# Kernel optimization log

Measured on AMD Instinct MI355X. Metric: run time of the kernel, lower is better.

## Reference

```python
import jax, jax.numpy as jnp
import numpy as np

TEMPERATURE = 0.07  # module init default
CHUNK = 2048        # row tile size, mirrors the triton tiling (never materialize full NxN)


def _normalize(x):
    # F.normalize(x, dim=1): x / max(||x||_2, eps)
    n = jnp.linalg.norm(x, axis=1, keepdims=True)
    return x / jnp.maximum(n, 1e-12)


def setup_inputs() -> dict:
    key = jax.random.key(0)
    k1, k2 = jax.random.split(key)
    N, D = 16384, 256
    return {
        "text_features": jax.random.normal(k1, (N, D), dtype=jnp.float32),
        "image_features": jax.random.normal(k2, (N, D), dtype=jnp.float32),
    }


def reference(text_features, image_features):
    X = _normalize(text_features)   # [N, D]
    Y = _normalize(image_features)  # [N, D]
    inv_t = 1.0 / TEMPERATURE
    n, d = X.shape
    Xc = X.reshape(n // CHUNK, CHUNK, d)

    def row_sum_exp(xc):
        # exp2(S*log2(e)/t - log2(e)/t) == exp((S - 1)/t); S = xc @ Y^T
        S = (jnp.einsum('id,jd->ij', xc, Y) - 1.0) * inv_t  # [CHUNK, N]
        return jnp.sum(jnp.exp(S), axis=1)                   # [CHUNK]

    # tiled accumulation of row-wise sum of exponentials (never holds NxN)
    sum_exp_row = jax.lax.map(row_sum_exp, Xc).reshape(n)   # [N]

    # diagonal (positive-pair) logits: Sv = (x_i . y_i - 1)/t
    Sv = (jnp.sum(X * Y, axis=1) - 1.0) * inv_t
    logits = jnp.log(jnp.exp(Sv) / sum_exp_row)
    return -jnp.mean(logits)
```

## Files before the change

kernel.cpp:

```cpp
#include <hip/hip_runtime.h>
#include <hip/hip_bf16.h>
#include <stdint.h>

#define D_DIM 256
#define INV_T 14.285714285714286f

#define BM 256
#define BN 256
#define BK 32
#define NSTEP (D_DIM / BK)

typedef __bf16 bf16x8 __attribute__((ext_vector_type(8)));
typedef float f32x16 __attribute__((ext_vector_type(16)));

__global__ __launch_bounds__(256) void lit_normalize(
    const float* __restrict__ X, const float* __restrict__ Y,
    __hip_bfloat16* __restrict__ Xb, __hip_bfloat16* __restrict__ Yb,
    float* __restrict__ Sv, float* __restrict__ rowsum)
{
    const int l = threadIdx.x & 63;
    const int row = blockIdx.x * 4 + (threadIdx.x >> 6);
    const size_t base = (size_t)row * D_DIM;
    const float4 x = ((const float4*)(X + base))[l];
    const float4 y = ((const float4*)(Y + base))[l];
    float nx = x.x * x.x + x.y * x.y + x.z * x.z + x.w * x.w;
    float ny = y.x * y.x + y.y * y.y + y.z * y.z + y.w * y.w;
    float dt = x.x * y.x + x.y * y.y + x.z * y.z + x.w * y.w;
    #pragma unroll
    for (int o = 1; o < 64; o <<= 1) {
        nx += __shfl_xor(nx, o);
        ny += __shfl_xor(ny, o);
        dt += __shfl_xor(dt, o);
    }
    const float ivx = 1.0f / fmaxf(sqrtf(nx), 1e-12f);
    const float ivy = 1.0f / fmaxf(sqrtf(ny), 1e-12f);

    __hip_bfloat16 hx0 = __float2bfloat16(x.x * ivx), hx1 = __float2bfloat16(x.y * ivx);
    __hip_bfloat16 hx2 = __float2bfloat16(x.z * ivx), hx3 = __float2bfloat16(x.w * ivx);
    __hip_bfloat16 hy0 = __float2bfloat16(y.x * ivy), hy1 = __float2bfloat16(y.y * ivy);
    __hip_bfloat16 hy2 = __float2bfloat16(y.z * ivy), hy3 = __float2bfloat16(y.w * ivy);
    ushort4 px, py;
    px.x = *(unsigned short*)&hx0; px.y = *(unsigned short*)&hx1;
    px.z = *(unsigned short*)&hx2; px.w = *(unsigned short*)&hx3;
    py.x = *(unsigned short*)&hy0; py.y = *(unsigned short*)&hy1;
    py.z = *(unsigned short*)&hy2; py.w = *(unsigned short*)&hy3;
    ((ushort4*)(Xb + base))[l] = px;
    ((ushort4*)(Yb + base))[l] = py;

    if (l == 0) {
        Sv[row] = (dt * ivx * ivy - 1.0f) * INV_T;
        rowsum[row] = 0.0f;
    }
}

__global__ __launch_bounds__(512, 2) void lit_gemm_rowsum(
    const __hip_bfloat16* __restrict__ Xb, const __hip_bfloat16* __restrict__ Yb,
    float* __restrict__ rowsum)
{
    __shared__ char lds[2 * 32768];

    const int tid = (int)threadIdx.x;
    const int l   = tid & 63;
    const int w   = tid >> 6;
    const int wi  = w >> 2;
    const int wj  = w & 3;

    const int nx  = (int)gridDim.x;
    const int bid = (int)blockIdx.y * nx + (int)blockIdx.x;
    const int cpx = (nx * (int)gridDim.y) >> 3;
    const int logical = (bid & 7) * cpx + (bid >> 3);
    const int bi = logical / nx;
    const int bj = logical % nx;
    const int iBase = bi * BM;
    const int jBase = bj * BN;

    f32x16 acc[2][4];
    #pragma unroll
    for (int a = 0; a < 2; ++a)
        #pragma unroll
        for (int b = 0; b < 4; ++b)
            #pragma unroll
            for (int r = 0; r < 16; ++r)
                acc[a][b][r] = 0.f;

    const int rq = l >> 2;
    const int sl = l & 3;
    const char* src[4];
    int dst[4];
    #pragma unroll
    for (int c = 0; c < 4; ++c) {
        const int g    = w * 4 + c;
        const int isY  = g >> 4;
        const int r16  = (g & 15) * 16;
        const int row  = r16 + rq;
        const int slot = sl ^ ((row >> 1) & 3);
        const char* base = isY ? (const char*)Yb + (size_t)jBase * (D_DIM * 2)
                               : (const char*)Xb + (size_t)iBase * (D_DIM * 2);
        src[c] = base + (size_t)row * (D_DIM * 2) + slot * 16;
        dst[c] = isY * 16384 + r16 * 64;
    }

#define STAGE(buf, t)                                                              \
    {                                                                              \
        _Pragma("unroll")                                                          \
        for (int c = 0; c < 4; ++c)                                                \
            __builtin_amdgcn_global_load_lds(                                      \
                (const __attribute__((address_space(1))) void*)(src[c] + (t) * (BK * 2)), \
                (__attribute__((address_space(3))) void*)(lds + (buf) * 32768 + dst[c]),  \
                16, 0, 0);                                                         \
    }

    STAGE(0, 0);
    __syncthreads();

    #pragma unroll
    for (int t = 0; t < NSTEP; ++t) {
        const char* Xs = lds + (t & 1) * 32768;
        const char* Ys = Xs + 16384;
        const int lr = l & 31;

        bf16x8 af[2][2], bg[2][4];
        #pragma unroll
        for (int kk = 0; kk < 2; ++kk) {
            const int sx = ((kk * 2 + (l >> 5)) ^ ((l >> 1) & 3)) * 16;
            af[kk][0] = *(const bf16x8*)(Ys + (wj * 64 +  0 + lr) * 64 + sx);
            af[kk][1] = *(const bf16x8*)(Ys + (wj * 64 + 32 + lr) * 64 + sx);
            bg[kk][0] = *(const bf16x8*)(Xs + (wi * 128 +  0 + lr) * 64 + sx);
            bg[kk][1] = *(const bf16x8*)(Xs + (wi * 128 + 32 + lr) * 64 + sx);
            bg[kk][2] = *(const bf16x8*)(Xs + (wi * 128 + 64 + lr) * 64 + sx);
            bg[kk][3] = *(const bf16x8*)(Xs + (wi * 128 + 96 + lr) * 64 + sx);
        }

        if (t < NSTEP - 1) STAGE((t + 1) & 1, t + 1);

        #pragma unroll
        for (int kk = 0; kk < 2; ++kk) {
            acc[0][0] = __builtin_amdgcn_mfma_f32_32x32x16_bf16(af[kk][0], bg[kk][0], acc[0][0], 0, 0, 0);
            acc[0][1] = __builtin_amdgcn_mfma_f32_32x32x16_bf16(af[kk][0], bg[kk][1], acc[0][1], 0, 0, 0);
            acc[0][2] = __builtin_amdgcn_mfma_f32_32x32x16_bf16(af[kk][0], bg[kk][2], acc[0][2], 0, 0, 0);
            acc[0][3] = __builtin_amdgcn_mfma_f32_32x32x16_bf16(af[kk][0], bg[kk][3], acc[0][3], 0, 0, 0);
            acc[1][0] = __builtin_amdgcn_mfma_f32_32x32x16_bf16(af[kk][1], bg[kk][0], acc[1][0], 0, 0, 0);
            acc[1][1] = __builtin_amdgcn_mfma_f32_32x32x16_bf16(af[kk][1], bg[kk][1], acc[1][1], 0, 0, 0);
            acc[1][2] = __builtin_amdgcn_mfma_f32_32x32x16_bf16(af[kk][1], bg[kk][2], acc[1][2], 0, 0, 0);
            acc[1][3] = __builtin_amdgcn_mfma_f32_32x32x16_bf16(af[kk][1], bg[kk][3], acc[1][3], 0, 0, 0);
        }

        __syncthreads();
    }

    float part[4];
    #pragma unroll
    for (int fi = 0; fi < 4; ++fi) {
        float s = 0.f;
        #pragma unroll
        for (int fj = 0; fj < 2; ++fj)
            #pragma unroll
            for (int r = 0; r < 16; ++r)
                s += __expf(fmaf(acc[fj][fi][r], INV_T, -INV_T));
        s += __shfl_xor(s, 32);
        part[fi] = s;
    }
    float (*rowpart4)[BM] = (float (*)[BM])lds;
    if (l < 32) {
        #pragma unroll
        for (int fi = 0; fi < 4; ++fi)
            rowpart4[wj][wi * 128 + fi * 32 + l] = part[fi];
    }
    __syncthreads();
    if (tid < BM) {
        const float v = rowpart4[0][tid] + rowpart4[1][tid]
                      + rowpart4[2][tid] + rowpart4[3][tid];
        atomicAdd(&rowsum[iBase + tid], v);
    }
}

__global__ __launch_bounds__(1024) void lit_finish(
    const float* __restrict__ Sv, const float* __restrict__ rowsum,
    float* __restrict__ out, int N)
{
    float s = 0.f;
    for (int i = threadIdx.x; i < N; i += 1024)
        s += Sv[i] - __logf(rowsum[i]);
    #pragma unroll
    for (int o = 1; o < 64; o <<= 1) s += __shfl_xor(s, o);
    __shared__ float sred[16];
    if ((threadIdx.x & 63) == 0) sred[threadIdx.x >> 6] = s;
    __syncthreads();
    if (threadIdx.x == 0) {
        float tot = 0.f;
        #pragma unroll
        for (int k = 0; k < 16; ++k) tot += sred[k];
        out[0] = -tot / (float)N;
    }
}

extern "C" void kernel_launch(void* const* d_in, const int* in_sizes, int n_in,
                              void* d_out, int out_size, void* d_ws, size_t ws_size,
                              hipStream_t stream)
{
    const float* X = (const float*)d_in[0];
    const float* Y = (const float*)d_in[1];
    const int N = in_sizes[0] / D_DIM;

    char* ws = (char*)d_ws;
    __hip_bfloat16* Xb = (__hip_bfloat16*)ws;
    __hip_bfloat16* Yb = (__hip_bfloat16*)(ws + (size_t)N * D_DIM * 2);
    float* Sv     = (float*)(ws + (size_t)N * D_DIM * 4);
    float* rowsum = (float*)(ws + (size_t)N * D_DIM * 4 + (size_t)N * 4);

    lit_normalize<<<N / 4, 256, 0, stream>>>(X, Y, Xb, Yb, Sv, rowsum);
    dim3 grid(N / BN, N / BM);
    lit_gemm_rowsum<<<grid, 512, 0, stream>>>(Xb, Yb, rowsum);
    lit_finish<<<1, 1024, 0, stream>>>(Sv, rowsum, (float*)d_out, N);
}
```

Baseline: 254.8 us.

## Switch GEMM to 128x128 tiles with 16x16x32 MFMA and single-buffered LDS

Rewrites the fused GEMM+rowsum kernel to use 128x128 output tiles, BK=64, 256 threads per block and 16x16x32 bf16 MFMA instructions, with a new XOR swizzle for 128-byte LDS rows. The double-buffered prefetch is replaced by a load-sync-compute-sync loop. The intent is higher occupancy (four blocks per CU) and more blocks for load balance. The cost is halved data reuse per tile, so more global/L2 traffic, and no overlap of loads with MFMA work.

```diff
diff --git a/kernel.cpp b/kernel.cpp
--- a/kernel.cpp
+++ b/kernel.cpp
@@ -5,13 +5,13 @@
 #define D_DIM 256
 #define INV_T 14.285714285714286f
 
-#define BM 256
-#define BN 256
-#define BK 32
+#define BM 128
+#define BN 128
+#define BK 64
 #define NSTEP (D_DIM / BK)
 
 typedef __bf16 bf16x8 __attribute__((ext_vector_type(8)));
-typedef float f32x16 __attribute__((ext_vector_type(16)));
+typedef float f32x4 __attribute__((ext_vector_type(4)));
 
 __global__ __launch_bounds__(256) void lit_normalize(
     const float* __restrict__ X, const float* __restrict__ Y,
@@ -53,17 +53,21 @@
     }
 }
 
-__global__ __launch_bounds__(512, 2) void lit_gemm_rowsum(
+__global__ __launch_bounds__(256, 4) void lit_gemm_rowsum(
     const __hip_bfloat16* __restrict__ Xb, const __hip_bfloat16* __restrict__ Yb,
     float* __restrict__ rowsum)
 {
-    __shared__ char lds[2 * 32768];
+    __shared__ char lds[2 * BM * BK * 2];
+    char* Xs = lds;
+    char* Ys = lds + BM * BK * 2;
 
     const int tid = (int)threadIdx.x;
     const int l   = tid & 63;
     const int w   = tid >> 6;
-    const int wi  = w >> 2;
-    const int wj  = w & 3;
+    const int wj  = w >> 1;
+    const int wi  = w & 1;
+    const int fr  = l & 15;
+    const int kg  = l >> 4;
 
     const int nx  = (int)gridDim.x;
     const int bid = (int)blockIdx.y * nx + (int)blockIdx.x;
@@ -74,104 +78,88 @@
     const int iBase = bi * BM;
     const int jBase = bj * BN;
 
-    f32x16 acc[2][4];
-    #pragma unroll
-    for (int a = 0; a < 2; ++a)
+    f32x4 acc[4][4];
+    const f32x4 zero = {0.f, 0.f, 0.f, 0.f};
+    #pragma unroll
+    for (int a = 0; a < 4; ++a)
         #pragma unroll
         for (int b = 0; b < 4; ++b)
-            #pragma unroll
-            for (int r = 0; r < 16; ++r)
-                acc[a][b][r] = 0.f;
-
-    const int rq = l >> 2;
-    const int sl = l & 3;
-    const char* src[4];
-    int dst[4];
-    #pragma unroll
-    for (int c = 0; c < 4; ++c) {
-        const int g    = w * 4 + c;
-        const int isY  = g >> 4;
-        const int r16  = (g & 15) * 16;
-        const int row  = r16 + rq;
-        const int slot = sl ^ ((row >> 1) & 3);
-        const char* base = isY ? (const char*)Yb + (size_t)jBase * (D_DIM * 2)
-                               : (const char*)Xb + (size_t)iBase * (D_DIM * 2);
-        src[c] = base + (size_t)row * (D_DIM * 2) + slot * 16;
-        dst[c] = isY * 16384 + r16 * 64;
-    }
-
-#define STAGE(buf, t)                                                              \
-    {                                                                              \
-        _Pragma("unroll")                                                          \
-        for (int c = 0; c < 4; ++c)                                                \
-            __builtin_amdgcn_global_load_lds(                                      \
-                (const __attribute__((address_space(1))) void*)(src[c] + (t) * (BK * 2)), \
-                (__attribute__((address_space(3))) void*)(lds + (buf) * 32768 + dst[c]),  \
-                16, 0, 0);                                                         \
-    }
-
-    STAGE(0, 0);
+            acc[a][b] = zero;
+
+    const int rq = l >> 3;
+    const int sl = l & 7;
+    const char* srcX[4]; const char* srcY[4];
+    int dstX[4], dstY[4];
+    #pragma unroll
+    for (int i = 0; i < 4; ++i) {
+        const int row  = w * 32 + i * 8 + rq;
+        const int slot = sl ^ (row & 7);
+        srcX[i] = (const char*)Xb + (size_t)(iBase + row) * (D_DIM * 2) + slot * 16;
+        srcY[i] = (const char*)Yb + (size_t)(jBase + row) * (D_DIM * 2) + slot * 16;
+        dstX[i] = (w * 32 + i * 8) * 128;
+        dstY[i] = BM * BK * 2 + (w * 32 + i * 8) * 128;
+    }
+
+    #pragma unroll
+    for (int t = 0; t < NSTEP; ++t) {
+        #pragma unroll
+        for (int i = 0; i < 4; ++i) {
+            __builtin_amdgcn_global_load_lds(
+                (const __attribute__((address_space(1))) void*)(srcX[i] + t * (BK * 2)),
+                (__attribute__((address_space(3))) void*)(lds + dstX[i]), 16, 0, 0);
+            __builtin_amdgcn_global_load_lds(
+                (const __attribute__((address_space(1))) void*)(srcY[i] + t * (BK * 2)),
+                (__attribute__((address_space(3))) void*)(lds + dstY[i]), 16, 0, 0);
+        }
+        __syncthreads();
+
+        #pragma unroll
+        for (int kk = 0; kk < 2; ++kk) {
+            bf16x8 af[4], bg[4];
+            #pragma unroll
+            for (int mj = 0; mj < 4; ++mj) {
+                const int row = wj * 64 + mj * 16 + fr;
+                const int sx  = ((kk * 4 + kg) ^ (row & 7)) * 16;
+                af[mj] = *(const bf16x8*)(Ys + row * 128 + sx);
+            }
+            #pragma unroll
+            for (int ni = 0; ni < 4; ++ni) {
+                const int row = wi * 64 + ni * 16 + fr;
+                const int sx  = ((kk * 4 + kg) ^ (row & 7)) * 16;
+                bg[ni] = *(const bf16x8*)(Xs + row * 128 + sx);
+            }
+            #pragma unroll
+            for (int mj = 0; mj < 4; ++mj)
+                #pragma unroll
+                for (int ni = 0; ni < 4; ++ni)
+                    acc[mj][ni] = __builtin_amdgcn_mfma_f32_16x16x32_bf16(
+                        af[mj], bg[ni], acc[mj][ni], 0, 0, 0);
+        }
+        __syncthreads();
+    }
+
+    float part[4];
+    #pragma unroll
+    for (int ni = 0; ni < 4; ++ni) {
+        float s = 0.f;
+        #pragma unroll
+        for (int mj = 0; mj < 4; ++mj)
+            #pragma unroll
+            for (int r = 0; r < 4; ++r)
+                s += __expf(fmaf(acc[mj][ni][r], INV_T, -INV_T));
+        s += __shfl_xor(s, 16);
+        s += __shfl_xor(s, 32);
+        part[ni] = s;
+    }
+    float (*rowpart2)[BM] = (float (*)[BM])lds;
+    if (l < 16) {
+        #pragma unroll
+        for (int ni = 0; ni < 4; ++ni)
+            rowpart2[wj][wi * 64 + ni * 16 + l] = part[ni];
+    }
     __syncthreads();
-
-    #pragma unroll
-    for (int t = 0; t < NSTEP; ++t) {
-        const char* Xs = lds + (t & 1) * 32768;
-        const char* Ys = Xs + 16384;
-        const int lr = l & 31;
-
-        bf16x8 af[2][2], bg[2][4];
-        #pragma unroll
-        for (int kk = 0; kk < 2; ++kk) {
-            const int sx = ((kk * 2 + (l >> 5)) ^ ((l >> 1) & 3)) * 16;
-            af[kk][0] = *(const bf16x8*)(Ys + (wj * 64 +  0 + lr) * 64 + sx);
-            af[kk][1] = *(const bf16x8*)(Ys + (wj * 64 + 32 + lr) * 64 + sx);
-            bg[kk][0] = *(const bf16x8*)(Xs + (wi * 128 +  0 + lr) * 64 + sx);
-            bg[kk][1] = *(const bf16x8*)(Xs + (wi * 128 + 32 + lr) * 64 + sx);
-            bg[kk][2] = *(const bf16x8*)(Xs + (wi * 128 + 64 + lr) * 64 + sx);
-            bg[kk][3] = *(const bf16x8*)(Xs + (wi * 128 + 96 + lr) * 64 + sx);
-        }
-
-        if (t < NSTEP - 1) STAGE((t + 1) & 1, t + 1);
-
-        #pragma unroll
-        for (int kk = 0; kk < 2; ++kk) {
-            acc[0][0] = __builtin_amdgcn_mfma_f32_32x32x16_bf16(af[kk][0], bg[kk][0], acc[0][0], 0, 0, 0);
-            acc[0][1] = __builtin_amdgcn_mfma_f32_32x32x16_bf16(af[kk][0], bg[kk][1], acc[0][1], 0, 0, 0);
-            acc[0][2] = __builtin_amdgcn_mfma_f32_32x32x16_bf16(af[kk][0], bg[kk][2], acc[0][2], 0, 0, 0);
-            acc[0][3] = __builtin_amdgcn_mfma_f32_32x32x16_bf16(af[kk][0], bg[kk][3], acc[0][3], 0, 0, 0);
-            acc[1][0] = __builtin_amdgcn_mfma_f32_32x32x16_bf16(af[kk][1], bg[kk][0], acc[1][0], 0, 0, 0);
-            acc[1][1] = __builtin_amdgcn_mfma_f32_32x32x16_bf16(af[kk][1], bg[kk][1], acc[1][1], 0, 0, 0);
-            acc[1][2] = __builtin_amdgcn_mfma_f32_32x32x16_bf16(af[kk][1], bg[kk][2], acc[1][2], 0, 0, 0);
-            acc[1][3] = __builtin_amdgcn_mfma_f32_32x32x16_bf16(af[kk][1], bg[kk][3], acc[1][3], 0, 0, 0);
-        }
-
-        __syncthreads();
-    }
-
-    float part[4];
-    #pragma unroll
-    for (int fi = 0; fi < 4; ++fi) {
-        float s = 0.f;
-        #pragma unroll
-        for (int fj = 0; fj < 2; ++fj)
-            #pragma unroll
-            for (int r = 0; r < 16; ++r)
-                s += __expf(fmaf(acc[fj][fi][r], INV_T, -INV_T));
-        s += __shfl_xor(s, 32);
-        part[fi] = s;
-    }
-    float (*rowpart4)[BM] = (float (*)[BM])lds;
-    if (l < 32) {
-        #pragma unroll
-        for (int fi = 0; fi < 4; ++fi)
-            rowpart4[wj][wi * 128 + fi * 32 + l] = part[fi];
-    }
-    __syncthreads();
-    if (tid < BM) {
-        const float v = rowpart4[0][tid] + rowpart4[1][tid]
-                      + rowpart4[2][tid] + rowpart4[3][tid];
-        atomicAdd(&rowsum[iBase + tid], v);
-    }
+    if (tid < BM)
+        atomicAdd(&rowsum[iBase + tid], rowpart2[0][tid] + rowpart2[1][tid]);
 }
 
 __global__ __launch_bounds__(1024) void lit_finish(
@@ -210,6 +198,6 @@
 
     lit_normalize<<<N / 4, 256, 0, stream>>>(X, Y, Xb, Yb, Sv, rowsum);
     dim3 grid(N / BN, N / BM);
-    lit_gemm_rowsum<<<grid, 512, 0, stream>>>(Xb, Yb, rowsum);
+    lit_gemm_rowsum<<<grid, 256, 0, stream>>>(Xb, Yb, rowsum);
     lit_finish<<<1, 1024, 0, stream>>>(Sv, rowsum, (float*)d_out, N);
 }
```

After: 230.7 us. 1.1x faster.
